# Performance work log

Measured on AMD Instinct MI355X. Metric: run time of the kernel, lower is better.

The kernel has to match this reference:

```python
import jax, jax.numpy as jnp
import numpy as np

D_MODEL = 1024
N_HEADS = 16
N_PHASE = 128
HEAD_DIM = D_MODEL // N_HEADS
PHASE_PER_HEAD = N_PHASE // N_HEADS
CONTENT_SCALE = 1.0 / np.sqrt(HEAD_DIM)
PHASE_SCALE = 1.0 / np.sqrt(PHASE_PER_HEAD)
LN_EPS = 1e-5


def create_position_phases(L, n_phase, base=10000.0):
    # RoPE-style: each freq repeated at even/odd indices (interleaved)
    inv_freq = 1.0 / base ** (jnp.arange(0, n_phase, 2, dtype=jnp.float32) / n_phase)
    pos = jnp.arange(L, dtype=jnp.float32)
    sinusoid = pos[:, None] * inv_freq[None, :]          # (L, n_phase//2)
    return jnp.repeat(sinusoid, 2, axis=1)               # (L, n_phase)


def setup_inputs() -> dict:
    key = jax.random.key(0)
    ks = jax.random.split(key, 12)
    B, L, D, P = 1, 2048, D_MODEL, N_PHASE
    s = 0.02
    return {
        'x_real': jax.random.normal(ks[0], (B, L, D), jnp.float32),
        'x_imag': jax.random.normal(ks[1], (B, L, D), jnp.float32),
        'Wq': jax.random.normal(ks[2], (D, D), jnp.float32) * s,
        'Wk': jax.random.normal(ks[3], (D, D), jnp.float32) * s,
        'Wv': jax.random.normal(ks[4], (D, D), jnp.float32) * s,
        'Wqp': jax.random.normal(ks[5], (D, P), jnp.float32) * s,
        'bqp': jax.random.uniform(ks[6], (P,), jnp.float32, -np.pi, np.pi),
        'Wkp': jax.random.normal(ks[7], (D, P), jnp.float32) * s,
        'bkp': jax.random.uniform(ks[8], (P,), jnp.float32, -np.pi, np.pi),
        'Wo': jax.random.normal(ks[9], (D, D), jnp.float32) * s,
        'alpha_logit': jnp.zeros((N_HEADS, 1, 1), jnp.float32),
        'ln_gamma': jnp.ones((D,), jnp.float32),
        'ln_beta': jnp.zeros((D,), jnp.float32),
    }


def _split_heads(x, B, L, H, hd):
    return x.reshape(B, L, H, hd).transpose(0, 2, 1, 3)  # (B,H,L,hd)


def reference(x_real, x_imag, Wq, Wk, Wv, Wqp, bqp, Wkp, bkp, Wo,
              alpha_logit, ln_gamma, ln_beta):
    B, L, D = x_real.shape
    H, hd, p = N_HEADS, HEAD_DIM, PHASE_PER_HEAD

    Q = _split_heads(x_real @ Wq, B, L, H, hd)
    K = _split_heads(x_real @ Wk, B, L, H, hd)
    V = _split_heads(x_real @ Wv, B, L, H, hd)
    content = jnp.einsum('bhqd,bhkd->bhqk', Q, K) * CONTENT_SCALE

    pos_phase = create_position_phases(L, N_PHASE)        # (L, P)
    Qt = _split_heads(x_imag @ Wqp + bqp + pos_phase, B, L, H, p)
    Kt = _split_heads(x_imag @ Wkp + bkp + pos_phase, B, L, H, p)
    phase = (jnp.einsum('bhqp,bhkp->bhqk', jnp.cos(Qt), jnp.cos(Kt))
             + jnp.einsum('bhqp,bhkp->bhqk', jnp.sin(Qt), jnp.sin(Kt))) * PHASE_SCALE

    alpha = jax.nn.sigmoid(alpha_logit)                   # (H,1,1) broadcasts over (B,H,L,L)
    scores = (1.0 - alpha) * content + alpha * phase

    causal = jnp.triu(jnp.ones((L, L), bool), 1)
    scores = jnp.where(causal, -jnp.inf, scores)
    attn = jax.nn.softmax(scores, axis=-1)

    out = jnp.einsum('bhqk,bhkd->bhqd', attn, V)
    out = out.transpose(0, 2, 1, 3).reshape(B, L, D) @ Wo

    h = x_real + out
    mu = jnp.mean(h, axis=-1, keepdims=True)
    var = jnp.var(h, axis=-1, keepdims=True)
    out_real = (h - mu) / jnp.sqrt(var + LN_EPS) * ln_gamma + ln_beta
    return out_real, x_imag
```

## Files before the change

### kernel.cpp

```cpp
#include <hip/hip_runtime.h>
#include <hip/hip_bf16.h>
#include <math.h>

#define L 2048
#define D 1024
#define NH 16
#define HD 64
#define P 128
#define HDE 96
#define CONTENT_SCALE 0.125f
#define PHASE_SCALE   0.35355339059327373f
#define VTS 72
#define PLS 72

typedef short bf16x8 __attribute__((ext_vector_type(8)));
typedef float f32x4 __attribute__((ext_vector_type(4)));

__device__ inline ushort f2b(float x) {
    __hip_bfloat16 b = __float2bfloat16(x);
    return *(ushort*)&b;
}
__device__ inline float b2f(ushort u) {
    unsigned v = (unsigned)u << 16;
    union { unsigned u; float f; } c; c.u = v; return c.f;
}

__device__ inline void sincos_hw(float ang, float* sn, float* cs) {
    float rev = ang * 0.15915494309189535f;
    rev -= floorf(rev);
    *sn = __builtin_amdgcn_sinf(rev);
    *cs = __builtin_amdgcn_cosf(rev);
}

__device__ inline void gld_lds16(const void* g, void* l) {
    __builtin_amdgcn_global_load_lds(
        (const __attribute__((address_space(1))) unsigned int*)g,
        (__attribute__((address_space(3))) unsigned int*)l,
        16, 0, 0);
}

__global__ void cvt2_kernel(const float4* __restrict__ sa, const float4* __restrict__ sb,
                            ushort4* __restrict__ da, ushort4* __restrict__ db, int n4) {
    const float4* src = blockIdx.y ? sb : sa;
    ushort4* dst = blockIdx.y ? db : da;
    int i = blockIdx.x * blockDim.x + threadIdx.x;
    if (i < n4) {
        float4 v = src[i];
        ushort4 o;
        o.x = f2b(v.x); o.y = f2b(v.y); o.z = f2b(v.z); o.w = f2b(v.w);
        dst[i] = o;
    }
}

__global__ void cvtw_kernel(const float* __restrict__ W0, const float* __restrict__ W1,
                            const float* __restrict__ W2, const float* __restrict__ W3,
                            const float* __restrict__ W4, const float* __restrict__ W5,
                            ushort* __restrict__ T0, ushort* __restrict__ T1,
                            ushort* __restrict__ T2, ushort* __restrict__ T3,
                            ushort* __restrict__ Tp) {
    const float* W; ushort* T; int ncols;
    switch (blockIdx.z) {
        case 0: W = W0; T = T0; ncols = D; break;
        case 1: W = W1; T = T1; ncols = D; break;
        case 2: W = W2; T = T2; ncols = D; break;
        case 3: W = W3; T = T3; ncols = D; break;
        case 4: W = W4; T = Tp; ncols = P; break;
        default: W = W5; T = Tp + (size_t)P * D; ncols = P; break;
    }
    int n0 = blockIdx.x * 32, k0 = blockIdx.y * 32;
    if (n0 >= ncols) return;
    __shared__ float tile[32][33];
    int tx = threadIdx.x, ty = threadIdx.y;
#pragma unroll
    for (int i = 0; i < 4; i++)
        tile[ty + i * 8][tx] = W[(size_t)(k0 + ty + i * 8) * ncols + n0 + tx];
    __syncthreads();
#pragma unroll
    for (int i = 0; i < 4; i++)
        T[(size_t)(n0 + ty + i * 8) * D + k0 + tx] = f2b(tile[tx][ty + i * 8]);
}

__global__ void zpad_kernel(ushort* __restrict__ Qe, ushort* __restrict__ Ke) {
    int i = blockIdx.x * blockDim.x + threadIdx.x;
    size_t base = (size_t)i * HDE + 80;
    uint4 z = make_uint4(0, 0, 0, 0);
    *(uint4*)(Qe + base) = z;
    *(uint4*)(Qe + base + 8) = z;
    *(uint4*)(Ke + base) = z;
    *(uint4*)(Ke + base + 8) = z;
}

__launch_bounds__(256)
__global__ void qkv_gemm(const ushort* __restrict__ Ab, const ushort* __restrict__ xib,
                         const ushort* __restrict__ Wtq, const ushort* __restrict__ Wtk,
                         const ushort* __restrict__ Wtv, const ushort* __restrict__ Wtp,
                         ushort* __restrict__ Qe, ushort* __restrict__ Ke,
                         ushort* __restrict__ Ve, const float* __restrict__ alpha,
                         const float* __restrict__ bqp, const float* __restrict__ bkp) {
    const int z = blockIdx.z;
    if (z == 3 && blockIdx.x >= 2) return;
    const ushort* At = (z == 3) ? xib : Ab;
    const ushort* Bt = (z == 0) ? Wtq : ((z == 1) ? Wtk : ((z == 2) ? Wtv : Wtp));
    __shared__ ushort As[128 * 32];
    __shared__ ushort Bs[128 * 32];
    const int tid = threadIdx.x;
    const int wave = tid >> 6, lane = tid & 63, quad = lane >> 4, ln16 = lane & 15;
    const int wm = wave >> 1, wn = wave & 1;
    const int m0 = blockIdx.y * 128, n0 = blockIdx.x * 128;
    f32x4 acc[4][4];
#pragma unroll
    for (int i = 0; i < 4; i++)
#pragma unroll
        for (int j = 0; j < 4; j++) acc[i][j] = (f32x4){0.f, 0.f, 0.f, 0.f};
    for (int kt = 0; kt < D; kt += 32) {
        __syncthreads();
#pragma unroll
        for (int i = 0; i < 2; i++) {
            int idx = i * 256 + tid;
            int row = idx >> 2, c8 = idx & 3;
            gld_lds16(At + (size_t)(m0 + row) * D + kt + c8 * 8, &As[idx * 8]);
            gld_lds16(Bt + (size_t)(n0 + row) * D + kt + c8 * 8, &Bs[idx * 8]);
        }
        __syncthreads();
        bf16x8 af[4], bfr[4];
#pragma unroll
        for (int t = 0; t < 4; t++) {
            af[t]  = *(const bf16x8*)(&As[(wm * 64 + t * 16 + ln16) * 32 + quad * 8]);
            bfr[t] = *(const bf16x8*)(&Bs[(wn * 64 + t * 16 + ln16) * 32 + quad * 8]);
        }
#pragma unroll
        for (int i = 0; i < 4; i++)
#pragma unroll
            for (int j = 0; j < 4; j++)
                acc[i][j] = __builtin_amdgcn_mfma_f32_16x16x32_bf16(af[i], bfr[j], acc[i][j], 0, 0, 0);
    }
    if (z < 3) {
        int hn = (n0 + wn * 64) >> 6;
        float s = 1.f;
        if (z == 0) s = (1.f - 1.f / (1.f + __expf(-alpha[hn]))) * CONTENT_SCALE;
        ushort* dst; int stride;
        if (z == 0)      { dst = Qe; stride = HDE; }
        else if (z == 1) { dst = Ke; stride = HDE; }
        else             { dst = Ve; stride = HD; }
#pragma unroll
        for (int i = 0; i < 4; i++)
#pragma unroll
            for (int j = 0; j < 4; j++) {
                int dcol = j * 16 + ln16;
#pragma unroll
                for (int r = 0; r < 4; r++) {
                    int m = m0 + wm * 64 + i * 16 + quad * 4 + r;
                    dst[((size_t)hn * L + m) * stride + dcol] = f2b(acc[i][j][r] * s);
                }
            }
    } else {
#pragma unroll
        for (int j = 0; j < 4; j++) {
            int cg = n0 + wn * 64 + j * 16 + ln16;
            int isQ = cg < P;
            int c = cg & (P - 1);
            int hh = c >> 3, jj = c & 7;
            float b = isQ ? bqp[c] : bkp[c];
            float sc = isQ ? (1.f / (1.f + __expf(-alpha[hh]))) * PHASE_SCALE : 1.f;
            float invf = __expf(-((float)(c & ~1) / 128.f) * 9.210340371976184f);
            ushort* dst = isQ ? Qe : Ke;
#pragma unroll
            for (int i = 0; i < 4; i++)
#pragma unroll
                for (int r = 0; r < 4; r++) {
                    int m = m0 + wm * 64 + i * 16 + quad * 4 + r;
                    float qt = acc[i][j][r] + b + (float)m * invf;
                    float sn, cs;
                    sincos_hw(qt, &sn, &cs);
                    size_t base = ((size_t)hh * L + m) * HDE;
                    dst[base + 64 + jj] = f2b(sc * cs);
                    dst[base + 72 + jj] = f2b(sc * sn);
                }
        }
    }
}

__launch_bounds__(256)
__global__ void wo_gemm(const ushort* __restrict__ Ab, const ushort* __restrict__ Bt,
                        float* __restrict__ C) {
    __shared__ ushort As[128 * 32];
    __shared__ ushort Bs[128 * 32];
    const int tid = threadIdx.x;
    const int wave = tid >> 6, lane = tid & 63, quad = lane >> 4, ln16 = lane & 15;
    const int wm = wave >> 1, wn = wave & 1;
    const int m0 = blockIdx.y * 128, n0 = blockIdx.x * 128;
    f32x4 acc[4][4];
#pragma unroll
    for (int i = 0; i < 4; i++)
#pragma unroll
        for (int j = 0; j < 4; j++) acc[i][j] = (f32x4){0.f, 0.f, 0.f, 0.f};
    for (int kt = 0; kt < D; kt += 32) {
        __syncthreads();
#pragma unroll
        for (int i = 0; i < 2; i++) {
            int idx = i * 256 + tid;
            int row = idx >> 2, c8 = idx & 3;
            gld_lds16(Ab + (size_t)(m0 + row) * D + kt + c8 * 8, &As[idx * 8]);
            gld_lds16(Bt + (size_t)(n0 + row) * D + kt + c8 * 8, &Bs[idx * 8]);
        }
        __syncthreads();
        bf16x8 af[4], bfr[4];
#pragma unroll
        for (int t = 0; t < 4; t++) {
            af[t]  = *(const bf16x8*)(&As[(wm * 64 + t * 16 + ln16) * 32 + quad * 8]);
            bfr[t] = *(const bf16x8*)(&Bs[(wn * 64 + t * 16 + ln16) * 32 + quad * 8]);
        }
#pragma unroll
        for (int i = 0; i < 4; i++)
#pragma unroll
            for (int j = 0; j < 4; j++)
                acc[i][j] = __builtin_amdgcn_mfma_f32_16x16x32_bf16(af[i], bfr[j], acc[i][j], 0, 0, 0);
    }
#pragma unroll
    for (int i = 0; i < 4; i++)
#pragma unroll
        for (int j = 0; j < 4; j++)
#pragma unroll
            for (int r = 0; r < 4; r++) {
                int m = m0 + wm * 64 + i * 16 + quad * 4 + r;
                int n = n0 + wn * 64 + j * 16 + ln16;
                C[(size_t)m * D + n] = acc[i][j][r];
            }
}

__launch_bounds__(256)
__global__ void flash_attn(const ushort* __restrict__ Qe, const ushort* __restrict__ Ke,
                           const ushort* __restrict__ Ve,
                           ushort* __restrict__ Opart, float* __restrict__ ml) {
    const int h = blockIdx.y;
    const int z = blockIdx.z;
    const int tid = threadIdx.x;
    const int wave = tid >> 6, lane = tid & 63, quad = lane >> 4, ln16 = lane & 15;
    const int cA = blockIdx.x, cB = 31 - blockIdx.x;
    const int hA = (cA + 2) >> 1, hB = (cB + 2) >> 1;
    const int startA = z ? hA : 0;
    const int nA = z ? (cA + 1 - hA) : hA;
    const int startB = z ? hB : 0;
    const int nB = z ? (cB + 1 - hB) : hB;
    const int ntot = nA + nB;

    ushort* Op = Opart + (size_t)z * L * D;
    float* mlp = ml + (size_t)z * NH * L;

    __shared__ ushort Kl[64 * HDE];
    __shared__ ushort Vt[HD * VTS];
    __shared__ ushort Pl[4][16 * PLS];

    const ushort* Kh  = Ke + (size_t)h * L * HDE;
    const ushort* Vh  = Ve + (size_t)h * L * HD;
    const ushort* Qh0 = Qe + (size_t)h * L * HDE;

    const int krow = tid & 63, dg = wave;

    bf16x8 onesv;
#pragma unroll
    for (int i = 0; i < 8; i++) onesv[i] = (short)0x3F80;

    if (nA == 0) {
        const int q0z = cA * 64 + wave * 16;
#pragma unroll
        for (int r = 0; r < 4; r++) {
            int q = q0z + quad * 4 + r;
            ushort* dst = Op + (size_t)q * D + h * HD;
#pragma unroll
            for (int nt = 0; nt < 4; nt++) dst[nt * 16 + ln16] = 0;
            if (ln16 == 0) mlp[(size_t)h * L + q] = 0.f;
        }
    }

    int t0 = (0 < nA) ? startA : startB;
    bf16x8 kreg[3], vreg[2];
    {
        const ushort* Ksrc = Kh + (size_t)(t0 * 64) * HDE;
#pragma unroll
        for (int ii = 0; ii < 3; ii++)
            kreg[ii] = *(const bf16x8*)(Ksrc + (size_t)(ii * 256 + tid) * 8);
#pragma unroll
        for (int i = 0; i < 2; i++)
            vreg[i] = *(const bf16x8*)(Vh + (size_t)(t0 * 64 + krow) * HD + dg * 16 + i * 8);
    }

    bf16x8 qa[3];
    f32x4 o[4], ol;

    for (int tt = 0; tt < ntot; tt++) {
        const int inB = (tt >= nA);
        const int c  = inB ? cB : cA;
        const int t  = inB ? startB + (tt - nA) : startA + tt;
        const int k0 = t * 64;
        const int q0 = c * 64 + wave * 16;

        __syncthreads();
#pragma unroll
        for (int ii = 0; ii < 3; ii++)
            *(bf16x8*)(&Kl[(ii * 256 + tid) * 8]) = kreg[ii];
#pragma unroll
        for (int i = 0; i < 2; i++)
#pragma unroll
            for (int jj = 0; jj < 8; jj++)
                Vt[(dg * 16 + i * 8 + jj) * VTS + krow] = (ushort)vreg[i][jj];
        __syncthreads();

        if (tt + 1 < ntot) {
            int inB2 = (tt + 1 >= nA);
            int t2 = inB2 ? startB + (tt + 1 - nA) : startA + tt + 1;
            int k02 = t2 * 64;
            const ushort* Ksrc = Kh + (size_t)k02 * HDE;
#pragma unroll
            for (int ii = 0; ii < 3; ii++)
                kreg[ii] = *(const bf16x8*)(Ksrc + (size_t)(ii * 256 + tid) * 8);
#pragma unroll
            for (int i = 0; i < 2; i++)
                vreg[i] = *(const bf16x8*)(Vh + (size_t)(k02 + krow) * HD + dg * 16 + i * 8);
        }

        if (tt == 0 || tt == nA) {
            const ushort* Qh = Qh0 + (size_t)q0 * HDE;
#pragma unroll
            for (int kc = 0; kc < 3; kc++)
                qa[kc] = *(const bf16x8*)(Qh + (size_t)ln16 * HDE + kc * 32 + quad * 8);
#pragma unroll
            for (int nt = 0; nt < 4; nt++) o[nt] = (f32x4){0.f, 0.f, 0.f, 0.f};
            ol = (f32x4){0.f, 0.f, 0.f, 0.f};
        }

        f32x4 s[4];
#pragma unroll
        for (int st = 0; st < 4; st++) s[st] = (f32x4){0.f, 0.f, 0.f, 0.f};
#pragma unroll
        for (int kc = 0; kc < 3; kc++)
#pragma unroll
            for (int st = 0; st < 4; st++) {
                bf16x8 kb = *(const bf16x8*)(&Kl[(st * 16 + ln16) * HDE + kc * 32 + quad * 8]);
                s[st] = __builtin_amdgcn_mfma_f32_16x16x32_bf16(qa[kc], kb, s[st], 0, 0, 0);
            }
        if (t == c) {
#pragma unroll
            for (int st = 0; st < 4; st++) {
                int key = k0 + st * 16 + ln16;
#pragma unroll
                for (int r = 0; r < 4; r++)
                    if (key > q0 + quad * 4 + r) s[st][r] = -1e30f;
            }
        }
#pragma unroll
        for (int st = 0; st < 4; st++)
#pragma unroll
            for (int r = 0; r < 4; r++)
                Pl[wave][(quad * 4 + r) * PLS + st * 16 + ln16] = f2b(__expf(s[st][r]));
        bf16x8 pa0 = *(const bf16x8*)(&Pl[wave][ln16 * PLS + quad * 8]);
        bf16x8 pa1 = *(const bf16x8*)(&Pl[wave][ln16 * PLS + 32 + quad * 8]);
#pragma unroll
        for (int nt = 0; nt < 4; nt++) {
            bf16x8 vb0 = *(const bf16x8*)(&Vt[(nt * 16 + ln16) * VTS + quad * 8]);
            bf16x8 vb1 = *(const bf16x8*)(&Vt[(nt * 16 + ln16) * VTS + 32 + quad * 8]);
            o[nt] = __builtin_amdgcn_mfma_f32_16x16x32_bf16(pa0, vb0, o[nt], 0, 0, 0);
            o[nt] = __builtin_amdgcn_mfma_f32_16x16x32_bf16(pa1, vb1, o[nt], 0, 0, 0);
        }
        ol = __builtin_amdgcn_mfma_f32_16x16x32_bf16(pa0, onesv, ol, 0, 0, 0);
        ol = __builtin_amdgcn_mfma_f32_16x16x32_bf16(pa1, onesv, ol, 0, 0, 0);

        if (tt == nA - 1 || tt == ntot - 1) {
#pragma unroll
            for (int r = 0; r < 4; r++) {
                int q = q0 + quad * 4 + r;
                ushort* dst = Op + (size_t)q * D + h * HD;
#pragma unroll
                for (int nt = 0; nt < 4; nt++)
                    dst[nt * 16 + ln16] = f2b(o[nt][r]);
                if (ln16 == 0) mlp[(size_t)h * L + q] = ol[r];
            }
        }
    }
}

__global__ void comb_kernel(const ushort* __restrict__ Opart, const float* __restrict__ ml,
                            ushort* __restrict__ AOb) {
    int q = blockIdx.x;
    int t = threadIdx.x;
    int h = t >> 4;
    float l0 = ml[(size_t)h * L + q];
    float l1 = ml[(size_t)NH * L + (size_t)h * L + q];
    float inv = 1.f / (l0 + l1);
    size_t idx = (size_t)q * D + t * 4;
    ushort4 a = *(const ushort4*)(Opart + idx);
    ushort4 b = *(const ushort4*)(Opart + (size_t)L * D + idx);
    ushort4 o;
    o.x = f2b((b2f(a.x) + b2f(b.x)) * inv);
    o.y = f2b((b2f(a.y) + b2f(b.y)) * inv);
    o.z = f2b((b2f(a.z) + b2f(b.z)) * inv);
    o.w = f2b((b2f(a.w) + b2f(b.w)) * inv);
    *(ushort4*)(AOb + idx) = o;
}

__global__ void ln_kernel(const float* __restrict__ xr, const float* __restrict__ o2,
                          const float* __restrict__ gamma, const float* __restrict__ beta,
                          float* __restrict__ outp, const float4* __restrict__ xi4,
                          float4* __restrict__ out1) {
    int l = blockIdx.x;
    int tid = threadIdx.x;
    int wave = tid >> 6;
    __shared__ float red[8];
    float hv[4];
    float s = 0.f;
#pragma unroll
    for (int i = 0; i < 4; i++) {
        int c = tid + i * 256;
        hv[i] = xr[(size_t)l * D + c] + o2[(size_t)l * D + c];
        s += hv[i];
    }
    out1[(size_t)l * (D / 4) + tid] = xi4[(size_t)l * (D / 4) + tid];
#pragma unroll
    for (int off = 1; off < 64; off <<= 1) s += __shfl_xor(s, off);
    if ((tid & 63) == 0) red[wave] = s;
    __syncthreads();
    float mu = (red[0] + red[1] + red[2] + red[3]) * (1.f / D);
    float v = 0.f;
#pragma unroll
    for (int i = 0; i < 4; i++) { float d = hv[i] - mu; v += d * d; }
#pragma unroll
    for (int off = 1; off < 64; off <<= 1) v += __shfl_xor(v, off);
    __syncthreads();
    if ((tid & 63) == 0) red[4 + wave] = v;
    __syncthreads();
    float rstd = rsqrtf((red[4] + red[5] + red[6] + red[7]) * (1.f / D) + 1e-5f);
#pragma unroll
    for (int i = 0; i < 4; i++) {
        int c = tid + i * 256;
        outp[(size_t)l * D + c] = (hv[i] - mu) * rstd * gamma[c] + beta[c];
    }
}

extern "C" void kernel_launch(void* const* d_in, const int* in_sizes, int n_in,
                              void* d_out, int out_size, void* d_ws, size_t ws_size,
                              hipStream_t stream) {
    const float* xr    = (const float*)d_in[0];
    const float* xi    = (const float*)d_in[1];
    const float* Wq    = (const float*)d_in[2];
    const float* Wk    = (const float*)d_in[3];
    const float* Wv    = (const float*)d_in[4];
    const float* Wqp   = (const float*)d_in[5];
    const float* bqp   = (const float*)d_in[6];
    const float* Wkp   = (const float*)d_in[7];
    const float* bkp   = (const float*)d_in[8];
    const float* Wo    = (const float*)d_in[9];
    const float* alpha = (const float*)d_in[10];
    const float* gamma = (const float*)d_in[11];
    const float* beta  = (const float*)d_in[12];

    const size_t LD = (size_t)L * D;
    const size_t MB = 1024 * 1024;

    char* A8 = (char*)d_out;
    char* B8 = A8 + LD * 4;
    ushort* xib = (ushort*)A8;
    ushort* AOb = (ushort*)A8;
    ushort* Wot = (ushort*)(A8 + 4 * MB);
    ushort* Wtq = (ushort*)(A8 + 6 * MB);
    ushort* xrb = (ushort*)B8;
    ushort* Wtk = (ushort*)(B8 + 4 * MB);
    ushort* Wtv = (ushort*)(B8 + 6 * MB);
    ushort* Opart = (ushort*)B8;
    float* outf = (float*)d_out;

    ushort* Qe = (ushort*)d_ws;
    ushort* Ke = Qe + (size_t)NH * L * HDE;
    ushort* Ve = Ke + (size_t)NH * L * HDE;
    ushort* Wqpkt = Ve + (size_t)NH * L * HD;
    float*  mlbuf = (float*)(Wqpkt + (size_t)256 * D);
    float*  O2 = (float*)d_ws;

    cvt2_kernel<<<dim3((int)(LD / 4 / 256), 2), 256, 0, stream>>>(
        (const float4*)xr, (const float4*)xi, (ushort4*)xrb, (ushort4*)xib, (int)(LD / 4));
    cvtw_kernel<<<dim3(32, 32, 6), dim3(32, 8), 0, stream>>>(
        Wq, Wk, Wv, Wo, Wqp, Wkp, Wtq, Wtk, Wtv, Wot, Wqpkt);
    zpad_kernel<<<NH * L / 256, 256, 0, stream>>>(Qe, Ke);

    qkv_gemm<<<dim3(8, 16, 4), 256, 0, stream>>>(xrb, xib, Wtq, Wtk, Wtv, Wqpkt,
                                                 Qe, Ke, Ve, alpha, bqp, bkp);

    flash_attn<<<dim3(16, NH, 2), 256, 0, stream>>>(Qe, Ke, Ve, Opart, mlbuf);

    comb_kernel<<<L, 256, 0, stream>>>(Opart, mlbuf, AOb);

    wo_gemm<<<dim3(8, 16), 256, 0, stream>>>(AOb, Wot, O2);

    ln_kernel<<<L, 256, 0, stream>>>(xr, O2, gamma, beta, outf,
                                     (const float4*)xi, (float4*)(B8));
}
```

Before: 206.9 us.

## Split attention KV range four ways with XCD-aware block mapping

Raises the flash-attention KV split from two to four partitions, launched as a flat 1024-block grid whose index is decoded so that blocks of the same head land on the same XCD, which should improve L2 reuse of K/V. The combine kernel now sums four bf16 partial outputs and four row sums. The partial buffer moves into the workspace. More blocks improve occupancy on the 256-CU device, at the cost of more partial-output traffic and a heavier combine step.

```diff
diff --git a/kernel.cpp b/kernel.cpp
--- a/kernel.cpp
+++ b/kernel.cpp
@@ -12,6 +12,7 @@
 #define PHASE_SCALE   0.35355339059327373f
 #define VTS 72
 #define PLS 72
+#define NSPLIT 4
 
 typedef short bf16x8 __attribute__((ext_vector_type(8)));
 typedef float f32x4 __attribute__((ext_vector_type(4)));
@@ -232,16 +233,17 @@
 __global__ void flash_attn(const ushort* __restrict__ Qe, const ushort* __restrict__ Ke,
                            const ushort* __restrict__ Ve,
                            ushort* __restrict__ Opart, float* __restrict__ ml) {
-    const int h = blockIdx.y;
-    const int z = blockIdx.z;
+    const int b = blockIdx.x;
+    const int xcd = b & 7;
+    const int r5 = b >> 3;
+    const int h = xcd * 2 + (r5 & 1);
+    const int cA = (r5 >> 1) & 15, cB = 31 - cA;
+    const int z = r5 >> 5;
     const int tid = threadIdx.x;
     const int wave = tid >> 6, lane = tid & 63, quad = lane >> 4, ln16 = lane & 15;
-    const int cA = blockIdx.x, cB = 31 - blockIdx.x;
-    const int hA = (cA + 2) >> 1, hB = (cB + 2) >> 1;
-    const int startA = z ? hA : 0;
-    const int nA = z ? (cA + 1 - hA) : hA;
-    const int startB = z ? hB : 0;
-    const int nB = z ? (cB + 1 - hB) : hB;
+    const int nTA = cA + 1, nTB = cB + 1;
+    const int sA = (z * nTA) >> 2, nA = (((z + 1) * nTA) >> 2) - sA;
+    const int sB = (z * nTB) >> 2, nB = (((z + 1) * nTB) >> 2) - sB;
     const int ntot = nA + nB;
 
     ushort* Op = Opart + (size_t)z * L * D;
@@ -273,7 +275,7 @@
         }
     }
 
-    int t0 = (0 < nA) ? startA : startB;
+    int t0 = (nA > 0) ? sA : sB;
     bf16x8 kreg[3], vreg[2];
     {
         const ushort* Ksrc = Kh + (size_t)(t0 * 64) * HDE;
@@ -291,7 +293,7 @@
     for (int tt = 0; tt < ntot; tt++) {
         const int inB = (tt >= nA);
         const int c  = inB ? cB : cA;
-        const int t  = inB ? startB + (tt - nA) : startA + tt;
+        const int t  = inB ? sB + (tt - nA) : sA + tt;
         const int k0 = t * 64;
         const int q0 = c * 64 + wave * 16;
 
@@ -308,7 +310,7 @@
 
         if (tt + 1 < ntot) {
             int inB2 = (tt + 1 >= nA);
-            int t2 = inB2 ? startB + (tt + 1 - nA) : startA + tt + 1;
+            int t2 = inB2 ? sB + (tt + 1 - nA) : sA + tt + 1;
             int k02 = t2 * 64;
             const ushort* Ksrc = Kh + (size_t)k02 * HDE;
 #pragma unroll
@@ -384,17 +386,21 @@
     int q = blockIdx.x;
     int t = threadIdx.x;
     int h = t >> 4;
-    float l0 = ml[(size_t)h * L + q];
-    float l1 = ml[(size_t)NH * L + (size_t)h * L + q];
-    float inv = 1.f / (l0 + l1);
+    float lsum = 0.f;
+#pragma unroll
+    for (int zz = 0; zz < NSPLIT; zz++)
+        lsum += ml[(size_t)zz * NH * L + (size_t)h * L + q];
+    float inv = 1.f / lsum;
     size_t idx = (size_t)q * D + t * 4;
-    ushort4 a = *(const ushort4*)(Opart + idx);
-    ushort4 b = *(const ushort4*)(Opart + (size_t)L * D + idx);
+    float ox = 0.f, oy = 0.f, oz = 0.f, ow = 0.f;
+#pragma unroll
+    for (int zz = 0; zz < NSPLIT; zz++) {
+        ushort4 a = *(const ushort4*)(Opart + (size_t)zz * L * D + idx);
+        ox += b2f(a.x); oy += b2f(a.y); oz += b2f(a.z); ow += b2f(a.w);
+    }
     ushort4 o;
-    o.x = f2b((b2f(a.x) + b2f(b.x)) * inv);
-    o.y = f2b((b2f(a.y) + b2f(b.y)) * inv);
-    o.z = f2b((b2f(a.z) + b2f(b.z)) * inv);
-    o.w = f2b((b2f(a.w) + b2f(b.w)) * inv);
+    o.x = f2b(ox * inv); o.y = f2b(oy * inv);
+    o.z = f2b(oz * inv); o.w = f2b(ow * inv);
     *(ushort4*)(AOb + idx) = o;
 }
 
@@ -465,14 +471,14 @@
     ushort* xrb = (ushort*)B8;
     ushort* Wtk = (ushort*)(B8 + 4 * MB);
     ushort* Wtv = (ushort*)(B8 + 6 * MB);
-    ushort* Opart = (ushort*)B8;
     float* outf = (float*)d_out;
 
     ushort* Qe = (ushort*)d_ws;
     ushort* Ke = Qe + (size_t)NH * L * HDE;
     ushort* Ve = Ke + (size_t)NH * L * HDE;
     ushort* Wqpkt = Ve + (size_t)NH * L * HD;
-    float*  mlbuf = (float*)(Wqpkt + (size_t)256 * D);
+    ushort* Opart = Wqpkt + (size_t)256 * D;
+    float*  mlbuf = (float*)(Opart + (size_t)NSPLIT * LD);
     float*  O2 = (float*)d_ws;
 
     cvt2_kernel<<<dim3((int)(LD / 4 / 256), 2), 256, 0, stream>>>(
@@ -484,7 +490,7 @@
     qkv_gemm<<<dim3(8, 16, 4), 256, 0, stream>>>(xrb, xib, Wtq, Wtk, Wtv, Wqpkt,
                                                  Qe, Ke, Ve, alpha, bqp, bkp);
 
-    flash_attn<<<dim3(16, NH, 2), 256, 0, stream>>>(Qe, Ke, Ve, Opart, mlbuf);
+    flash_attn<<<1024, 256, 0, stream>>>(Qe, Ke, Ve, Opart, mlbuf);
 
     comb_kernel<<<L, 256, 0, stream>>>(Opart, mlbuf, AOb);
 
```

Result: faster. 202.2 us (-2.3%).
